# Kernel tuning notes

Hardware: AMD Instinct MI355X
Metric: run time of the kernel (lower is better)

Reference implementation:

```python
import jax, jax.numpy as jnp
import numpy as np
from jax import lax

K = 1024          # number_embeddings
D = 256           # embedding_dimension
BETA = 0.25


def setup_inputs() -> dict:
    key = jax.random.key(0)
    k1, k2 = jax.random.split(key)
    z = jax.random.normal(k1, (32, 32, 32, D), dtype=jnp.float32)
    # codebook initialized uniform in [-1/K, 1/K] as in the original layer
    codebook = jax.random.uniform(k2, (K, D), dtype=jnp.float32,
                                  minval=-1.0 / K, maxval=1.0 / K)
    return {"z": z, "codebook": codebook}


def reference(z, codebook):
    # z: [B, H, W, D] -> flatten to [N, D]
    zf = z.reshape(-1, D)
    # squared-distance matrix [N, K]: ||z||^2 + ||e||^2 - 2 z e^T
    d = ((zf * zf).sum(axis=1, keepdims=True)
         + (codebook * codebook).sum(axis=1)[None, :]
         - 2.0 * (zf @ codebook.T))
    idx = jnp.argmin(d, axis=1)                      # [N]
    quantized = codebook[idx].reshape(z.shape)       # gather + reshape

    commitment_loss = BETA * jnp.mean((lax.stop_gradient(quantized) - z) ** 2)
    # straight-through estimator
    quantized_ste = z + lax.stop_gradient(quantized - z)

    # perplexity from empirical code usage (scatter-add instead of NxK one-hot)
    n = zf.shape[0]
    avg_probs = jnp.zeros((K,), dtype=zf.dtype).at[idx].add(1.0) / n
    perplexity = jnp.exp(-jnp.sum(avg_probs * jnp.log(avg_probs + 1e-10)))

    return quantized_ste, idx, jnp.zeros((), dtype=z.dtype), commitment_loss, perplexity
```

## Files before the change

kernel.cpp:

```cpp
#include <hip/hip_runtime.h>

#define N_ROWS 32768
#define DIM 256
#define KCODES 1024

#define Q_N (N_ROWS * DIM)
#define IDX_OFF Q_N
#define ZERO_OFF (Q_N + N_ROWS)
#define LOSS_OFF (ZERO_OFF + 1)
#define PERP_OFF (ZERO_OFF + 2)

#define AMBIG_S  0.12f

#define TC 64
#define HALF_TILES 8
#define PAIR_GRID 768
#define FULL_GRID 1024
#define GATHER_BLOCKS 1024
#define GATHER_ITERS 8

typedef __attribute__((ext_vector_type(8))) _Float16 f16x8;
typedef __attribute__((ext_vector_type(4))) float f32x4;
typedef unsigned short u16;
typedef unsigned long long u64;


__device__ inline u16 f16bits(_Float16 h) {
    union { _Float16 h; u16 u; } x; x.h = h; return x.u;
}

__device__ inline bool lexless(float av, int ai, float bv, int bi) {
    return av < bv || (av == bv && ai < bi);
}

typedef __attribute__((address_space(3))) unsigned int as3_uint;
typedef __attribute__((address_space(1))) const unsigned int as1_uint;
__device__ inline void gload_lds16(const void* g, void* l) {
    __builtin_amdgcn_global_load_lds((as1_uint*)g, (as3_uint*)l, 16, 0, 0);
}

__global__ __launch_bounds__(256) void vq_prep_cb(const float* __restrict__ cb,
                                                  float* __restrict__ sen,
                                                  u16* __restrict__ e16,
                                                  unsigned* __restrict__ hist,
                                                  unsigned* __restrict__ pcnt,
                                                  unsigned* __restrict__ fcnt) {
    int b = blockIdx.x, t = threadIdx.x;
    if (b < 4) {
        hist[b * 256 + t] = 0u;
        if (b == 0 && t == 0) { *pcnt = 0u; *fcnt = 0u; }
    }
    int code = b * 4 + (t >> 6);
    int lane = t & 63;
    size_t eoff = (size_t)code * DIM + lane * 4;
    float4 v = *(const float4*)(cb + eoff);
    double s = (double)v.x * v.x + (double)v.y * v.y + (double)v.z * v.z + (double)v.w * v.w;
    #pragma unroll
    for (int off = 32; off; off >>= 1) s += __shfl_down(s, off, 64);
    if (lane == 0) sen[code] = (float)s;
    ushort4 us;
    us.x = f16bits((_Float16)(-1024.0f * v.x));
    us.y = f16bits((_Float16)(-1024.0f * v.y));
    us.z = f16bits((_Float16)(-1024.0f * v.z));
    us.w = f16bits((_Float16)(-1024.0f * v.w));
    *(ushort4*)(e16 + eoff) = us;
}

__global__ __launch_bounds__(256, 2) void vq_mfma(const float* __restrict__ z,
                                                  const u16* __restrict__ e16,
                                                  const float* __restrict__ sen,
                                                  unsigned* __restrict__ cand) {
    __shared__ char lds[2][32768];
    const int tid = threadIdx.x;
    const int wid = tid >> 6;
    const int lane = tid & 63;
    const int col16 = lane & 15;
    const int koct = lane >> 4;
    const int s3 = col16 & 7;
    const int rowblk = blockIdx.x & 255;
    const int half = blockIdx.x >> 8;
    const int rowbase = rowblk * 128 + wid * 32;

    f16x8 zf[2][8];
    #pragma unroll
    for (int g = 0; g < 2; ++g) {
        const float* zp = z + (size_t)(rowbase + g * 16 + col16) * DIM + koct * 8;
        #pragma unroll
        for (int dc = 0; dc < 8; ++dc) {
            float4 f0 = *(const float4*)(zp + dc * 32);
            float4 f1 = *(const float4*)(zp + dc * 32 + 4);
            f16x8 h;
            h[0] = (_Float16)f0.x; h[1] = (_Float16)f0.y;
            h[2] = (_Float16)f0.z; h[3] = (_Float16)f0.w;
            h[4] = (_Float16)f1.x; h[5] = (_Float16)f1.y;
            h[6] = (_Float16)f1.z; h[7] = (_Float16)f1.w;
            zf[g][dc] = h;
        }
    }

    unsigned k1[2][4], k2[2][4], k3[2][4];
    #pragma unroll
    for (int g = 0; g < 2; ++g)
        #pragma unroll
        for (int r = 0; r < 4; ++r) { k1[g][r] = k2[g][r] = k3[g][r] = 0xFFFFFFFFu; }

    auto STAGE = [&](int tt, int b) {
        #pragma unroll
        for (int r = 0; r < 8; ++r) {
            int p = r * 256 + tid;
            int src = p ^ ((p >> 5) & 7);
            const char* sp = (const char*)e16 + (size_t)half * 262144
                             + (size_t)tt * 32768 + src * 16;
            gload_lds16(sp, &lds[b][p * 16]);
        }
    };

    STAGE(0, 0);
    __syncthreads();

    for (int tt = 0; tt < HALF_TILES; ++tt) {
        if (tt + 1 < HALF_TILES) STAGE(tt + 1, (tt + 1) & 1);
        const char* bb = lds[tt & 1];
        f32x4 acc[2][4];
        #pragma unroll
        for (int ct = 0; ct < 4; ++ct) {
            float sv = sen[half * 512 + tt * TC + ct * 16 + col16];
            float b0 = fmaf(512.0f, sv, 512.0f);
            acc[0][ct] = (f32x4){b0, b0, b0, b0};
            acc[1][ct] = (f32x4){b0, b0, b0, b0};
        }
        #pragma unroll
        for (int dc = 0; dc < 8; ++dc) {
            int swcol = ((dc * 4 + koct) ^ s3) * 16;
            #pragma unroll
            for (int ct = 0; ct < 4; ++ct) {
                int off = (ct * 16 + col16) * 512 + swcol;
                f16x8 bv = *(const f16x8*)(bb + off);
                acc[0][ct] = __builtin_amdgcn_mfma_f32_16x16x32_f16(zf[0][dc], bv, acc[0][ct], 0, 0, 0);
                acc[1][ct] = __builtin_amdgcn_mfma_f32_16x16x32_f16(zf[1][dc], bv, acc[1][ct], 0, 0, 0);
            }
        }
        #pragma unroll
        for (int ct = 0; ct < 4; ++ct) {
            const unsigned lidx = (unsigned)(tt * 4 + ct);
            #pragma unroll
            for (int g = 0; g < 2; ++g)
                #pragma unroll
                for (int r = 0; r < 4; ++r) {
                    float s = acc[g][ct][r];
                    unsigned key = (__float_as_uint(s) & 0xFFFFFFC0u) | lidx;
                    unsigned o1 = k1[g][r];
                    k1[g][r] = min(o1, key);
                    k3[g][r] = min(k3[g][r], max(k2[g][r], key));
                    k2[g][r] = min(max(key, o1), k2[g][r]);
                }
        }
        __syncthreads();
    }

    #pragma unroll
    for (int g = 0; g < 2; ++g)
        #pragma unroll
        for (int r = 0; r < 4; ++r) {
            float a1 = __uint_as_float(k1[g][r] & 0xFFFFFFC0u);
            float a2 = __uint_as_float(k2[g][r] & 0xFFFFFFC0u);
            float a3 = __uint_as_float(k3[g][r] & 0xFFFFFFC0u);
            int l1 = (int)(k1[g][r] & 63u), l2 = (int)(k2[g][r] & 63u), l3 = (int)(k3[g][r] & 63u);
            int b1 = half * 512 + (l1 >> 2) * TC + (l1 & 3) * 16 + col16;
            int b2 = half * 512 + (l2 >> 2) * TC + (l2 & 3) * 16 + col16;
            int b3 = half * 512 + (l3 >> 2) * TC + (l3 & 3) * 16 + col16;
            #pragma unroll
            for (int m = 1; m < 16; m <<= 1) {
                float o1 = __shfl_xor(a1, m, 64), o2 = __shfl_xor(a2, m, 64), o3 = __shfl_xor(a3, m, 64);
                int p1 = __shfl_xor(b1, m, 64), p2 = __shfl_xor(b2, m, 64), p3 = __shfl_xor(b3, m, 64);
                #pragma unroll
                for (int k = 0; k < 3; ++k) {
                    float ov = (k == 0) ? o1 : (k == 1) ? o2 : o3;
                    int oi = (k == 0) ? p1 : (k == 1) ? p2 : p3;
                    if (lexless(ov, oi, a1, b1)) {
                        a3 = a2; b3 = b2; a2 = a1; b2 = b1; a1 = ov; b1 = oi;
                    } else if (lexless(ov, oi, a2, b2)) {
                        a3 = a2; b3 = b2; a2 = ov; b2 = oi;
                    } else if (lexless(ov, oi, a3, b3)) {
                        a3 = ov; b3 = oi;
                    }
                }
            }
            if (col16 == 0) {
                int row = rowbase + g * 16 + koct * 4 + r;
                unsigned* cp = cand + ((size_t)half * N_ROWS + row) * 6;
                cp[0] = __float_as_uint(a1); cp[1] = (unsigned)b1;
                cp[2] = __float_as_uint(a2); cp[3] = (unsigned)b2;
                cp[4] = __float_as_uint(a3); cp[5] = (unsigned)b3;
            }
        }
}

__global__ __launch_bounds__(256) void vq_merge(const unsigned* __restrict__ cand,
                                                float* __restrict__ idx_out,
                                                unsigned* __restrict__ pcnt,
                                                uint2* __restrict__ pairlist,
                                                unsigned* __restrict__ fcnt,
                                                unsigned* __restrict__ fulllist,
                                                u64* __restrict__ fullkey) {
    int row = blockIdx.x * 256 + threadIdx.x;
    const unsigned* cA = cand + (size_t)row * 6;
    const unsigned* cB = cand + ((size_t)N_ROWS + row) * 6;
    float a1 = __uint_as_float(cA[0]), a2 = __uint_as_float(cA[2]), a3 = __uint_as_float(cA[4]);
    int   b1 = (int)cA[1], b2 = (int)cA[3], b3 = (int)cA[5];
    float o1 = __uint_as_float(cB[0]), o2 = __uint_as_float(cB[2]), o3 = __uint_as_float(cB[4]);
    int   p1 = (int)cB[1], p2 = (int)cB[3], p3 = (int)cB[5];
    #pragma unroll
    for (int k = 0; k < 3; ++k) {
        float ov = (k == 0) ? o1 : (k == 1) ? o2 : o3;
        int oi = (k == 0) ? p1 : (k == 1) ? p2 : p3;
        if (lexless(ov, oi, a1, b1)) {
            a3 = a2; b3 = b2; a2 = a1; b2 = b1; a1 = ov; b1 = oi;
        } else if (lexless(ov, oi, a2, b2)) {
            a3 = a2; b3 = b2; a2 = ov; b2 = oi;
        } else if (lexless(ov, oi, a3, b3)) {
            a3 = ov; b3 = oi;
        }
    }
    idx_out[row] = (float)b1;
    if (a2 - a1 < AMBIG_S) {
        if (a3 - a1 < AMBIG_S) {
            unsigned slot = atomicAdd(fcnt, 1u);
            fulllist[slot] = (unsigned)row;
            fullkey[slot] = ~0ull;
        } else {
            unsigned slot = atomicAdd(pcnt, 1u);
            pairlist[slot] = make_uint2((unsigned)row,
                                        ((unsigned)b1 << 16) | (unsigned)b2);
        }
    }
}

__device__ inline float szn_wave(const float* __restrict__ zrow, int lane) {
    int sub = lane & 15;
    int hb = sub >> 3;
    int j = sub & 7;
    const float* a = zrow + hb * 128 + j;
    float v0 = a[0];
    float c = __fmul_rn(v0, v0);
    #pragma unroll
    for (int i = 1; i < 16; ++i) {
        float w = a[8 * i];
        c = __fadd_rn(c, __fmul_rn(w, w));
    }
    float p;
    p = __shfl_xor(c, 1, 64); c = __fadd_rn(c, p);
    p = __shfl_xor(c, 2, 64); c = __fadd_rn(c, p);
    p = __shfl_xor(c, 4, 64); c = __fadd_rn(c, p);
    p = __shfl_xor(c, 8, 64); c = __fadd_rn(c, p);
    return c;
}

__global__ __launch_bounds__(256) void vq_fixpair(const float* __restrict__ z,
                                                  const float* __restrict__ cb,
                                                  const float* __restrict__ sen,
                                                  const unsigned* __restrict__ pcnt,
                                                  const uint2* __restrict__ pairlist,
                                                  float* __restrict__ idx_out) {
    int wave = blockIdx.x * 4 + (threadIdx.x >> 6);
    int lane = threadIdx.x & 63;
    int half = lane >> 5, s5 = lane & 31;
    int n = (int)*pcnt;
    for (int w = wave; w < n; w += PAIR_GRID * 4) {
        uint2 pr = pairlist[w];
        int row = (int)pr.x;
        int c1 = (int)(pr.y >> 16), c2 = (int)(pr.y & 0xffffu);
        const float* zrow = z + (size_t)row * DIM;
        float sz = szn_wave(zrow, lane);
        int c = half ? c2 : c1;
        const float* zp = zrow + s5 * 8;
        const float* ep = cb + (size_t)c * DIM + s5 * 8;
        float4 za = *(const float4*)zp, zb = *(const float4*)(zp + 4);
        float4 ea = *(const float4*)ep, eb = *(const float4*)(ep + 4);
        double acc = (double)ea.x * za.x + (double)ea.y * za.y
                   + (double)ea.z * za.z + (double)ea.w * za.w
                   + (double)eb.x * zb.x + (double)eb.y * zb.y
                   + (double)eb.z * zb.z + (double)eb.w * zb.w;
        #pragma unroll
        for (int m = 1; m < 32; m <<= 1) acc += __shfl_xor(acc, m, 64);
        double d2 = __shfl(acc, 32, 64);
        if (lane == 0) {
            float A1 = __fadd_rn(sz, sen[c1]);
            float dref1 = __fmaf_rn(-2.0f, (float)acc, A1);
            float A2 = __fadd_rn(sz, sen[c2]);
            float dref2 = __fmaf_rn(-2.0f, (float)d2, A2);
            int win = lexless(dref1, c1, dref2, c2) ? c1 : c2;
            idx_out[row] = (float)win;
        }
    }
}

__global__ __launch_bounds__(64) void vq_fixfull(const float* __restrict__ z,
                                                 const float* __restrict__ cb,
                                                 const float* __restrict__ sen,
                                                 const unsigned* __restrict__ fcnt,
                                                 const unsigned* __restrict__ fulllist,
                                                 u64* __restrict__ fullkey) {
    __shared__ float et[64 * 257];
    __shared__ float zs[DIM];
    const int t = threadIdx.x;
    unsigned nitems = (*fcnt) * 16u;
    for (unsigned item = blockIdx.x; item < nitems; item += FULL_GRID) {
        int slot = (int)(item >> 4);
        int row = (int)fulllist[slot];
        int c0 = (int)(item & 15u) * 64;
        #pragma unroll 8
        for (int i = 0; i < 64; ++i) {
            int g4 = i * 64 + t;
            int code = g4 >> 6, d0 = (g4 & 63) * 4;
            float4 v = *(const float4*)(cb + (size_t)(c0 + code) * DIM + d0);
            int base = code * 257 + d0;
            et[base] = v.x; et[base + 1] = v.y; et[base + 2] = v.z; et[base + 3] = v.w;
        }
        {
            float4 v = *(const float4*)(z + (size_t)row * DIM + t * 4);
            zs[t * 4] = v.x; zs[t * 4 + 1] = v.y; zs[t * 4 + 2] = v.z; zs[t * 4 + 3] = v.w;
        }
        __syncthreads();
        float sz = szn_wave(zs, t);
        const int rb = t * 257;
        double a0 = 0.0, a1 = 0.0, a2 = 0.0, a3 = 0.0;
        #pragma unroll 16
        for (int d = 0; d < DIM; d += 4) {
            a0 += (double)et[rb + d]     * (double)zs[d];
            a1 += (double)et[rb + d + 1] * (double)zs[d + 1];
            a2 += (double)et[rb + d + 2] * (double)zs[d + 2];
            a3 += (double)et[rb + d + 3] * (double)zs[d + 3];
        }
        double dot = (a0 + a1) + (a2 + a3);
        int c = c0 + t;
        float A = __fadd_rn(sz, sen[c]);
        float dref = __fmaf_rn(-2.0f, (float)dot, A);
        float bv = dref; int bi = c;
        #pragma unroll
        for (int m = 1; m < 64; m <<= 1) {
            float ov = __shfl_xor(bv, m, 64);
            int oi = __shfl_xor(bi, m, 64);
            if (lexless(ov, oi, bv, bi)) { bv = ov; bi = oi; }
        }
        if (t == 0) {
            u64 key = ((u64)__float_as_uint(bv) << 32) | (unsigned)bi;
            atomicMin(&fullkey[slot], key);
        }
        __syncthreads();
    }
}

__global__ __launch_bounds__(256) void vq_resolve(const unsigned* __restrict__ fcnt,
                                                  const unsigned* __restrict__ fulllist,
                                                  const u64* __restrict__ fullkey,
                                                  float* __restrict__ idx_out) {
    int n = (int)*fcnt;
    for (int i = threadIdx.x; i < n; i += 256)
        idx_out[fulllist[i]] = (float)(unsigned)(fullkey[i] & 0xFFFFFFFFu);
}

__global__ __launch_bounds__(256) void vq_gather(const float* __restrict__ z,
                                                 const float* __restrict__ cb,
                                                 const float* __restrict__ idxf,
                                                 float* __restrict__ qout,
                                                 unsigned* __restrict__ hist,
                                                 double* __restrict__ partials) {
    const int tid = threadIdx.x;
    double lacc = 0.0;
    #pragma unroll
    for (int it = 0; it < GATHER_ITERS; ++it) {
        int g = it * (GATHER_BLOCKS * 256) + blockIdx.x * 256 + tid;
        int row = g >> 6, c4 = g & 63;
        int idx = (int)idxf[row];
        if (c4 == 0) atomicAdd(&hist[idx], 1u);
        float4 zv = *(const float4*)(z + (size_t)g * 4);
        float4 qv = *(const float4*)(cb + (size_t)idx * DIM + c4 * 4);
        float dx = qv.x - zv.x, dy = qv.y - zv.y, dz = qv.z - zv.z, dw = qv.w - zv.w;
        float4 o;
        o.x = zv.x + dx; o.y = zv.y + dy; o.z = zv.z + dz; o.w = zv.w + dw;
        *(float4*)(qout + (size_t)g * 4) = o;
        lacc += (double)(dx * dx + dy * dy + dz * dz + dw * dw);
    }
    #pragma unroll
    for (int off = 32; off; off >>= 1) lacc += __shfl_down(lacc, off, 64);
    __shared__ double wsum[4];
    int lane = tid & 63, wv = tid >> 6;
    if (lane == 0) wsum[wv] = lacc;
    __syncthreads();
    if (tid == 0)
        partials[blockIdx.x] = (wsum[0] + wsum[1]) + (wsum[2] + wsum[3]);
}

__global__ __launch_bounds__(1024) void vq_finalize(const unsigned* __restrict__ hist,
                                                    const double* __restrict__ partials,
                                                    float* __restrict__ out) {
    __shared__ float red[1024];
    __shared__ double redd[1024];
    int t = threadIdx.x;
    float p = (float)hist[t] * (1.0f / (float)N_ROWS);
    red[t] = p * logf(p + 1e-10f);
    redd[t] = partials[t];
    __syncthreads();
    for (int s = 512; s; s >>= 1) {
        if (t < s) { red[t] += red[t + s]; redd[t] += redd[t + s]; }
        __syncthreads();
    }
    if (t == 0) {
        out[ZERO_OFF] = 0.0f;
        out[LOSS_OFF] = (float)(0.25 * redd[0] / (double)Q_N);
        out[PERP_OFF] = expf(-red[0]);
    }
}

extern "C" void kernel_launch(void* const* d_in, const int* in_sizes, int n_in,
                              void* d_out, int out_size, void* d_ws, size_t ws_size,
                              hipStream_t stream) {
    const float* z = (const float*)d_in[0];
    const float* cb = (const float*)d_in[1];
    float* out = (float*)d_out;

    float* sen = (float*)d_ws;
    unsigned* hist = (unsigned*)((char*)d_ws + 4096);
    unsigned* pcnt = (unsigned*)((char*)d_ws + 8192);
    unsigned* fcnt = (unsigned*)((char*)d_ws + 8196);
    uint2* pairlist = (uint2*)((char*)d_ws + 8448);
    unsigned* fulllist = (unsigned*)((char*)d_ws + 270592);
    u16* e16 = (u16*)((char*)d_ws + 401664);
    double* partials = (double*)((char*)d_ws + 925952);
    u64* fullkey = (u64*)((char*)d_ws + 934144);
    unsigned* cand = (unsigned*)((char*)d_ws + 1196288);

    vq_prep_cb<<<KCODES / 4, 256, 0, stream>>>(cb, sen, e16, hist, pcnt, fcnt);
    vq_mfma<<<512, 256, 0, stream>>>(z, e16, sen, cand);
    vq_merge<<<N_ROWS / 256, 256, 0, stream>>>(cand, out + IDX_OFF,
                                               pcnt, pairlist, fcnt, fulllist, fullkey);
    vq_fixpair<<<PAIR_GRID, 256, 0, stream>>>(z, cb, sen, pcnt, pairlist, out + IDX_OFF);
    vq_fixfull<<<FULL_GRID, 64, 0, stream>>>(z, cb, sen, fcnt, fulllist, fullkey);
    vq_resolve<<<1, 256, 0, stream>>>(fcnt, fulllist, fullkey, out + IDX_OFF);
    vq_gather<<<GATHER_BLOCKS, 256, 0, stream>>>(z, cb, out + IDX_OFF, out, hist, partials);
    vq_finalize<<<1, 1024, 0, stream>>>(hist, partials, out);
}
```

Baseline: 105.8 us.

## Split codebook search into quarters with smaller tiles and higher occupancy

The MFMA distance kernel now splits the codebook four ways instead of two, using 32-code tiles and half the LDS, and launches twice as many blocks with a higher occupancy hint. The merge kernel combines four top-3 candidate lists per row instead of two. The candidate buffer moves from the workspace into the output buffer, which is later overwritten by the gather. The aim is more parallelism and latency hiding, at the cost of loading z twice as often, more per-tile key overhead, and more candidate traffic.

```diff
diff --git a/kernel.cpp b/kernel.cpp
--- a/kernel.cpp
+++ b/kernel.cpp
@@ -12,8 +12,8 @@
 
 #define AMBIG_S  0.12f
 
-#define TC 64
-#define HALF_TILES 8
+#define TC 32
+#define QT 8
 #define PAIR_GRID 768
 #define FULL_GRID 1024
 #define GATHER_BLOCKS 1024
@@ -66,11 +66,11 @@
     *(ushort4*)(e16 + eoff) = us;
 }
 
-__global__ __launch_bounds__(256, 2) void vq_mfma(const float* __restrict__ z,
+__global__ __launch_bounds__(256, 4) void vq_mfma(const float* __restrict__ z,
                                                   const u16* __restrict__ e16,
                                                   const float* __restrict__ sen,
                                                   unsigned* __restrict__ cand) {
-    __shared__ char lds[2][32768];
+    __shared__ char lds[2][16384];
     const int tid = threadIdx.x;
     const int wid = tid >> 6;
     const int lane = tid & 63;
@@ -78,7 +78,7 @@
     const int koct = lane >> 4;
     const int s3 = col16 & 7;
     const int rowblk = blockIdx.x & 255;
-    const int half = blockIdx.x >> 8;
+    const int quarter = blockIdx.x >> 8;
     const int rowbase = rowblk * 128 + wid * 32;
 
     f16x8 zf[2][8];
@@ -106,11 +106,11 @@
 
     auto STAGE = [&](int tt, int b) {
         #pragma unroll
-        for (int r = 0; r < 8; ++r) {
+        for (int r = 0; r < 4; ++r) {
             int p = r * 256 + tid;
             int src = p ^ ((p >> 5) & 7);
-            const char* sp = (const char*)e16 + (size_t)half * 262144
-                             + (size_t)tt * 32768 + src * 16;
+            const char* sp = (const char*)e16 + (size_t)quarter * 131072
+                             + (size_t)tt * 16384 + src * 16;
             gload_lds16(sp, &lds[b][p * 16]);
         }
     };
@@ -118,13 +118,13 @@
     STAGE(0, 0);
     __syncthreads();
 
-    for (int tt = 0; tt < HALF_TILES; ++tt) {
-        if (tt + 1 < HALF_TILES) STAGE(tt + 1, (tt + 1) & 1);
+    for (int tt = 0; tt < QT; ++tt) {
+        if (tt + 1 < QT) STAGE(tt + 1, (tt + 1) & 1);
         const char* bb = lds[tt & 1];
-        f32x4 acc[2][4];
-        #pragma unroll
-        for (int ct = 0; ct < 4; ++ct) {
-            float sv = sen[half * 512 + tt * TC + ct * 16 + col16];
+        f32x4 acc[2][2];
+        #pragma unroll
+        for (int ct = 0; ct < 2; ++ct) {
+            float sv = sen[quarter * 256 + tt * TC + ct * 16 + col16];
             float b0 = fmaf(512.0f, sv, 512.0f);
             acc[0][ct] = (f32x4){b0, b0, b0, b0};
             acc[1][ct] = (f32x4){b0, b0, b0, b0};
@@ -133,7 +133,7 @@
         for (int dc = 0; dc < 8; ++dc) {
             int swcol = ((dc * 4 + koct) ^ s3) * 16;
             #pragma unroll
-            for (int ct = 0; ct < 4; ++ct) {
+            for (int ct = 0; ct < 2; ++ct) {
                 int off = (ct * 16 + col16) * 512 + swcol;
                 f16x8 bv = *(const f16x8*)(bb + off);
                 acc[0][ct] = __builtin_amdgcn_mfma_f32_16x16x32_f16(zf[0][dc], bv, acc[0][ct], 0, 0, 0);
@@ -141,8 +141,8 @@
             }
         }
         #pragma unroll
-        for (int ct = 0; ct < 4; ++ct) {
-            const unsigned lidx = (unsigned)(tt * 4 + ct);
+        for (int ct = 0; ct < 2; ++ct) {
+            const unsigned lidx = (unsigned)(tt * 2 + ct);
             #pragma unroll
             for (int g = 0; g < 2; ++g)
                 #pragma unroll
@@ -166,9 +166,9 @@
             float a2 = __uint_as_float(k2[g][r] & 0xFFFFFFC0u);
             float a3 = __uint_as_float(k3[g][r] & 0xFFFFFFC0u);
             int l1 = (int)(k1[g][r] & 63u), l2 = (int)(k2[g][r] & 63u), l3 = (int)(k3[g][r] & 63u);
-            int b1 = half * 512 + (l1 >> 2) * TC + (l1 & 3) * 16 + col16;
-            int b2 = half * 512 + (l2 >> 2) * TC + (l2 & 3) * 16 + col16;
-            int b3 = half * 512 + (l3 >> 2) * TC + (l3 & 3) * 16 + col16;
+            int b1 = quarter * 256 + (l1 >> 1) * TC + (l1 & 1) * 16 + col16;
+            int b2 = quarter * 256 + (l2 >> 1) * TC + (l2 & 1) * 16 + col16;
+            int b3 = quarter * 256 + (l3 >> 1) * TC + (l3 & 1) * 16 + col16;
             #pragma unroll
             for (int m = 1; m < 16; m <<= 1) {
                 float o1 = __shfl_xor(a1, m, 64), o2 = __shfl_xor(a2, m, 64), o3 = __shfl_xor(a3, m, 64);
@@ -188,7 +188,7 @@
             }
             if (col16 == 0) {
                 int row = rowbase + g * 16 + koct * 4 + r;
-                unsigned* cp = cand + ((size_t)half * N_ROWS + row) * 6;
+                unsigned* cp = cand + ((size_t)quarter * N_ROWS + row) * 6;
                 cp[0] = __float_as_uint(a1); cp[1] = (unsigned)b1;
                 cp[2] = __float_as_uint(a2); cp[3] = (unsigned)b2;
                 cp[4] = __float_as_uint(a3); cp[5] = (unsigned)b3;
@@ -204,22 +204,25 @@
                                                 unsigned* __restrict__ fulllist,
                                                 u64* __restrict__ fullkey) {
     int row = blockIdx.x * 256 + threadIdx.x;
-    const unsigned* cA = cand + (size_t)row * 6;
-    const unsigned* cB = cand + ((size_t)N_ROWS + row) * 6;
-    float a1 = __uint_as_float(cA[0]), a2 = __uint_as_float(cA[2]), a3 = __uint_as_float(cA[4]);
-    int   b1 = (int)cA[1], b2 = (int)cA[3], b3 = (int)cA[5];
-    float o1 = __uint_as_float(cB[0]), o2 = __uint_as_float(cB[2]), o3 = __uint_as_float(cB[4]);
-    int   p1 = (int)cB[1], p2 = (int)cB[3], p3 = (int)cB[5];
-    #pragma unroll
-    for (int k = 0; k < 3; ++k) {
-        float ov = (k == 0) ? o1 : (k == 1) ? o2 : o3;
-        int oi = (k == 0) ? p1 : (k == 1) ? p2 : p3;
-        if (lexless(ov, oi, a1, b1)) {
-            a3 = a2; b3 = b2; a2 = a1; b2 = b1; a1 = ov; b1 = oi;
-        } else if (lexless(ov, oi, a2, b2)) {
-            a3 = a2; b3 = b2; a2 = ov; b2 = oi;
-        } else if (lexless(ov, oi, a3, b3)) {
-            a3 = ov; b3 = oi;
+    const unsigned* c0 = cand + (size_t)row * 6;
+    float a1 = __uint_as_float(c0[0]), a2 = __uint_as_float(c0[2]), a3 = __uint_as_float(c0[4]);
+    int   b1 = (int)c0[1], b2 = (int)c0[3], b3 = (int)c0[5];
+    #pragma unroll
+    for (int q = 1; q < 4; ++q) {
+        const unsigned* cq = cand + ((size_t)q * N_ROWS + row) * 6;
+        float o1 = __uint_as_float(cq[0]), o2 = __uint_as_float(cq[2]), o3 = __uint_as_float(cq[4]);
+        int   p1 = (int)cq[1], p2 = (int)cq[3], p3 = (int)cq[5];
+        #pragma unroll
+        for (int k = 0; k < 3; ++k) {
+            float ov = (k == 0) ? o1 : (k == 1) ? o2 : o3;
+            int oi = (k == 0) ? p1 : (k == 1) ? p2 : p3;
+            if (lexless(ov, oi, a1, b1)) {
+                a3 = a2; b3 = b2; a2 = a1; b2 = b1; a1 = ov; b1 = oi;
+            } else if (lexless(ov, oi, a2, b2)) {
+                a3 = a2; b3 = b2; a2 = ov; b2 = oi;
+            } else if (lexless(ov, oi, a3, b3)) {
+                a3 = ov; b3 = oi;
+            }
         }
     }
     idx_out[row] = (float)b1;
@@ -429,10 +432,10 @@
     u16* e16 = (u16*)((char*)d_ws + 401664);
     double* partials = (double*)((char*)d_ws + 925952);
     u64* fullkey = (u64*)((char*)d_ws + 934144);
-    unsigned* cand = (unsigned*)((char*)d_ws + 1196288);
+    unsigned* cand = (unsigned*)d_out;
 
     vq_prep_cb<<<KCODES / 4, 256, 0, stream>>>(cb, sen, e16, hist, pcnt, fcnt);
-    vq_mfma<<<512, 256, 0, stream>>>(z, e16, sen, cand);
+    vq_mfma<<<1024, 256, 0, stream>>>(z, e16, sen, cand);
     vq_merge<<<N_ROWS / 256, 256, 0, stream>>>(cand, out + IDX_OFF,
                                                pcnt, pairlist, fcnt, fulllist, fullkey);
     vq_fixpair<<<PAIR_GRID, 256, 0, stream>>>(z, cb, sen, pcnt, pairlist, out + IDX_OFF);
```

Result: slower. 123.5 us (+16.7%).

## Pre-swizzle codebook into MFMA fragment order and load B directly from global

Applied to the files above, without the earlier changes.

The prep kernel now writes the fp16 codebook in the exact per-lane fragment order the MFMA loop consumes, so each lane reads a contiguous 16-byte chunk. The distance kernel drops the LDS double buffer, the global-to-LDS async loads and the per-tile barriers, and reads B fragments straight from global memory (hitting L2) with the tile loop unrolled by two. This removes LDS traffic and synchronisation, but every wave now refetches the codebook from cache independently, which raises cache bandwidth demand and exposes load latency to the MFMA chain.

```diff
diff --git a/kernel.cpp b/kernel.cpp
--- a/kernel.cpp
+++ b/kernel.cpp
@@ -33,15 +33,9 @@
     return av < bv || (av == bv && ai < bi);
 }
 
-typedef __attribute__((address_space(3))) unsigned int as3_uint;
-typedef __attribute__((address_space(1))) const unsigned int as1_uint;
-__device__ inline void gload_lds16(const void* g, void* l) {
-    __builtin_amdgcn_global_load_lds((as1_uint*)g, (as3_uint*)l, 16, 0, 0);
-}
-
 __global__ __launch_bounds__(256) void vq_prep_cb(const float* __restrict__ cb,
                                                   float* __restrict__ sen,
-                                                  u16* __restrict__ e16,
+                                                  u16* __restrict__ eswz,
                                                   unsigned* __restrict__ hist,
                                                   unsigned* __restrict__ pcnt,
                                                   unsigned* __restrict__ fcnt) {
@@ -50,33 +44,50 @@
         hist[b * 256 + t] = 0u;
         if (b == 0 && t == 0) { *pcnt = 0u; *fcnt = 0u; }
     }
-    int code = b * 4 + (t >> 6);
-    int lane = t & 63;
-    size_t eoff = (size_t)code * DIM + lane * 4;
-    float4 v = *(const float4*)(cb + eoff);
-    double s = (double)v.x * v.x + (double)v.y * v.y + (double)v.z * v.z + (double)v.w * v.w;
-    #pragma unroll
-    for (int off = 32; off; off >>= 1) s += __shfl_down(s, off, 64);
-    if (lane == 0) sen[code] = (float)s;
-    ushort4 us;
-    us.x = f16bits((_Float16)(-1024.0f * v.x));
-    us.y = f16bits((_Float16)(-1024.0f * v.y));
-    us.z = f16bits((_Float16)(-1024.0f * v.z));
-    us.w = f16bits((_Float16)(-1024.0f * v.w));
-    *(ushort4*)(e16 + eoff) = us;
+    {
+        int code = b * 4 + (t >> 6);
+        int lane = t & 63;
+        float4 v = *(const float4*)(cb + (size_t)code * DIM + lane * 4);
+        double s = (double)v.x * v.x + (double)v.y * v.y + (double)v.z * v.z + (double)v.w * v.w;
+        #pragma unroll
+        for (int off = 32; off; off >>= 1) s += __shfl_down(s, off, 64);
+        if (lane == 0) sen[code] = (float)s;
+    }
+    if (t < 128) {
+        int g = b * 128 + t;
+        int lane = g & 63;
+        int ct = (g >> 6) & 3;
+        int dc = (g >> 8) & 7;
+        int tt = (g >> 11) & 7;
+        int half = g >> 14;
+        int code = half * 512 + tt * TC + ct * 16 + (lane & 15);
+        int d0 = dc * 32 + (lane >> 4) * 8;
+        const float* src = cb + (size_t)code * DIM + d0;
+        float4 f0 = *(const float4*)src;
+        float4 f1 = *(const float4*)(src + 4);
+        ushort4 lo, hi;
+        lo.x = f16bits((_Float16)(-1024.0f * f0.x));
+        lo.y = f16bits((_Float16)(-1024.0f * f0.y));
+        lo.z = f16bits((_Float16)(-1024.0f * f0.z));
+        lo.w = f16bits((_Float16)(-1024.0f * f0.w));
+        hi.x = f16bits((_Float16)(-1024.0f * f1.x));
+        hi.y = f16bits((_Float16)(-1024.0f * f1.y));
+        hi.z = f16bits((_Float16)(-1024.0f * f1.z));
+        hi.w = f16bits((_Float16)(-1024.0f * f1.w));
+        *(ushort4*)(eswz + (size_t)g * 8) = lo;
+        *(ushort4*)(eswz + (size_t)g * 8 + 4) = hi;
+    }
 }
 
 __global__ __launch_bounds__(256, 2) void vq_mfma(const float* __restrict__ z,
-                                                  const u16* __restrict__ e16,
+                                                  const u16* __restrict__ eswz,
                                                   const float* __restrict__ sen,
                                                   unsigned* __restrict__ cand) {
-    __shared__ char lds[2][32768];
     const int tid = threadIdx.x;
     const int wid = tid >> 6;
     const int lane = tid & 63;
     const int col16 = lane & 15;
     const int koct = lane >> 4;
-    const int s3 = col16 & 7;
     const int rowblk = blockIdx.x & 255;
     const int half = blockIdx.x >> 8;
     const int rowbase = rowblk * 128 + wid * 32;
@@ -104,23 +115,10 @@
         #pragma unroll
         for (int r = 0; r < 4; ++r) { k1[g][r] = k2[g][r] = k3[g][r] = 0xFFFFFFFFu; }
 
-    auto STAGE = [&](int tt, int b) {
-        #pragma unroll
-        for (int r = 0; r < 8; ++r) {
-            int p = r * 256 + tid;
-            int src = p ^ ((p >> 5) & 7);
-            const char* sp = (const char*)e16 + (size_t)half * 262144
-                             + (size_t)tt * 32768 + src * 16;
-            gload_lds16(sp, &lds[b][p * 16]);
-        }
-    };
-
-    STAGE(0, 0);
-    __syncthreads();
-
+    const u16* fb = eswz + (size_t)half * 16384 * 8 + (size_t)lane * 8;
+
+    #pragma unroll 2
     for (int tt = 0; tt < HALF_TILES; ++tt) {
-        if (tt + 1 < HALF_TILES) STAGE(tt + 1, (tt + 1) & 1);
-        const char* bb = lds[tt & 1];
         f32x4 acc[2][4];
         #pragma unroll
         for (int ct = 0; ct < 4; ++ct) {
@@ -131,11 +129,9 @@
         }
         #pragma unroll
         for (int dc = 0; dc < 8; ++dc) {
-            int swcol = ((dc * 4 + koct) ^ s3) * 16;
             #pragma unroll
             for (int ct = 0; ct < 4; ++ct) {
-                int off = (ct * 16 + col16) * 512 + swcol;
-                f16x8 bv = *(const f16x8*)(bb + off);
+                f16x8 bv = *(const f16x8*)(fb + ((size_t)tt * 2048 + dc * 256 + ct * 64) * 8);
                 acc[0][ct] = __builtin_amdgcn_mfma_f32_16x16x32_f16(zf[0][dc], bv, acc[0][ct], 0, 0, 0);
                 acc[1][ct] = __builtin_amdgcn_mfma_f32_16x16x32_f16(zf[1][dc], bv, acc[1][ct], 0, 0, 0);
             }
@@ -155,7 +151,6 @@
                     k2[g][r] = min(max(key, o1), k2[g][r]);
                 }
         }
-        __syncthreads();
     }
 
     #pragma unroll
@@ -426,13 +421,13 @@
     unsigned* fcnt = (unsigned*)((char*)d_ws + 8196);
     uint2* pairlist = (uint2*)((char*)d_ws + 8448);
     unsigned* fulllist = (unsigned*)((char*)d_ws + 270592);
-    u16* e16 = (u16*)((char*)d_ws + 401664);
+    u16* eswz = (u16*)((char*)d_ws + 401664);
     double* partials = (double*)((char*)d_ws + 925952);
     u64* fullkey = (u64*)((char*)d_ws + 934144);
     unsigned* cand = (unsigned*)((char*)d_ws + 1196288);
 
-    vq_prep_cb<<<KCODES / 4, 256, 0, stream>>>(cb, sen, e16, hist, pcnt, fcnt);
-    vq_mfma<<<512, 256, 0, stream>>>(z, e16, sen, cand);
+    vq_prep_cb<<<KCODES / 4, 256, 0, stream>>>(cb, sen, eswz, hist, pcnt, fcnt);
+    vq_mfma<<<512, 256, 0, stream>>>(z, eswz, sen, cand);
     vq_merge<<<N_ROWS / 256, 256, 0, stream>>>(cand, out + IDX_OFF,
                                                pcnt, pairlist, fcnt, fulllist, fullkey);
     vq_fixpair<<<PAIR_GRID, 256, 0, stream>>>(z, cb, sen, pcnt, pairlist, out + IDX_OFF);
```

Result: slower. 163.3 us (+54.3%).
